# Optimization experiments

Measured on AMD Instinct MI355X. Metric: run time of the kernel, lower is better.

The kernel has to match this reference:

```python
import jax, jax.numpy as jnp
import numpy as np

B, S, D, H = 4, 2048, 1024, 16
HD = D // H  # head dim = 64


def setup_inputs() -> dict:
    key = jax.random.key(0)
    ks = jax.random.split(key, 11)
    scale = 1.0 / np.sqrt(D)
    return {
        "q": jax.random.normal(ks[0], (B, S, D), jnp.float32),
        "k": jax.random.normal(ks[1], (B, S, D), jnp.float32),
        "v": jax.random.normal(ks[2], (B, S, D), jnp.float32),
        "w_q": jax.random.normal(ks[3], (D, D), jnp.float32) * scale,
        "b_q": jax.random.normal(ks[4], (D,), jnp.float32) * scale,
        "w_k": jax.random.normal(ks[5], (D, D), jnp.float32) * scale,
        "b_k": jax.random.normal(ks[6], (D,), jnp.float32) * scale,
        "w_v": jax.random.normal(ks[7], (D, D), jnp.float32) * scale,
        "b_v": jax.random.normal(ks[8], (D,), jnp.float32) * scale,
        "w_o": jax.random.normal(ks[9], (D, D), jnp.float32) * scale,
        "b_o": jax.random.normal(ks[10], (D,), jnp.float32) * scale,
    }


def _split_heads(x):
    # [B,S,D] -> [B,H,S,HD]
    return x.reshape(B, S, H, HD).transpose(0, 2, 1, 3)


def reference(q, k, v, w_q, b_q, w_k, b_k, w_v, b_v, w_o, b_o):
    qh = _split_heads(q @ w_q + b_q)
    kh = _split_heads(k @ w_k + b_k)
    vh = _split_heads(v @ w_v + b_v)
    # full score matrix [B,H,S,S], as in the naive torch code
    score = jnp.einsum("bhqd,bhkd->bhqk", qh, kh) / jnp.sqrt(jnp.float32(HD))
    attn = jax.nn.softmax(score, axis=-1)
    out = jnp.einsum("bhqk,bhkd->bhqd", attn, vh)
    out = out.transpose(0, 2, 1, 3).reshape(B, S, D)
    return out @ w_o + b_o
```

## Files before the change

### kernel.cpp

```cpp
#include <hip/hip_runtime.h>
#include <hip/hip_bf16.h>

#define BB 4
#define SS 2048
#define DD 1024
#define HH 16
#define HDD 64
#define MM (BB*SS)

using bf16x8 = __attribute__((ext_vector_type(8))) short;
using f32x4  = __attribute__((ext_vector_type(4))) float;
using f32x16 = __attribute__((ext_vector_type(16))) float;

static __device__ __forceinline__ ushort f2bf(float f) {
    __hip_bfloat16 h = __float2bfloat16(f);
    return *reinterpret_cast<ushort*>(&h);
}

static __device__ __forceinline__ void gload_lds16(const ushort* g, ushort* l) {
    __builtin_amdgcn_global_load_lds(
        (const __attribute__((address_space(1))) unsigned int*)g,
        (__attribute__((address_space(3))) unsigned int*)l, 16, 0, 0);
}

static __device__ __forceinline__ unsigned cvtpk(float lo, float hi) {
    unsigned r;
    asm("v_cvt_pk_bf16_f32 %0, %1, %2" : "=v"(r) : "v"(lo), "v"(hi));
    return r;
}

static __device__ __forceinline__ float exp2_raw(float x) {
    float r;
    asm("v_exp_f32 %0, %1" : "=v"(r) : "v"(x));
    return r;
}

static __device__ __forceinline__ void halfswap(unsigned& a, unsigned& b, int hi) {
#if __has_builtin(__builtin_amdgcn_permlane32_swap)
    typedef int v2i __attribute__((ext_vector_type(2)));
    v2i r = __builtin_amdgcn_permlane32_swap((int)a, (int)b, false, false);
    a = (unsigned)r.x; b = (unsigned)r.y;
#else
    unsigned xa = (unsigned)__shfl_xor((int)a, 32);
    unsigned xb = (unsigned)__shfl_xor((int)b, 32);
    unsigned na = hi ? xb : a;
    unsigned nb = hi ? b : xa;
    a = na; b = nb;
#endif
}

#define PIPE_BAR(N) do {                                          \
    asm volatile("s_waitcnt vmcnt(" #N ")" ::: "memory");         \
    __builtin_amdgcn_sched_barrier(0);                            \
    __builtin_amdgcn_s_barrier();                                 \
    __builtin_amdgcn_sched_barrier(0);                            \
} while (0)

__global__ __launch_bounds__(256) void wtrans_k(
    const float* __restrict__ w0, const float* __restrict__ w1,
    const float* __restrict__ w2, const float* __restrict__ w3,
    ushort* __restrict__ o0, ushort* __restrict__ o1,
    ushort* __restrict__ o2, ushort* __restrict__ o3)
{
    __shared__ float tile[32][33];
    const float* W; ushort* O;
    switch (blockIdx.z) {
        case 0:  W = w0; O = o0; break;
        case 1:  W = w1; O = o1; break;
        case 2:  W = w2; O = o2; break;
        default: W = w3; O = o3; break;
    }
    const int tx = threadIdx.x & 31, ty = threadIdx.x >> 5;
    const int n0 = blockIdx.x * 32, k0 = blockIdx.y * 32;
    #pragma unroll
    for (int i = 0; i < 4; i++)
        tile[ty * 4 + i][tx] = W[(size_t)(k0 + ty * 4 + i) * DD + n0 + tx];
    __syncthreads();
    #pragma unroll
    for (int i = 0; i < 4; i++)
        O[(size_t)(n0 + ty * 4 + i) * DD + k0 + tx] = f2bf(tile[tx][ty * 4 + i]);
}

__global__ __launch_bounds__(256) void gemm_qkv_k(
    const float* __restrict__ qi, const float* __restrict__ ki,
    const float* __restrict__ vi,
    const ushort* __restrict__ wqT, const ushort* __restrict__ wkT,
    const ushort* __restrict__ wvT,
    const float* __restrict__ b_q, const float* __restrict__ b_k,
    const float* __restrict__ b_v,
    ushort* __restrict__ qo, ushort* __restrict__ ko, ushort* __restrict__ vo)
{
    __shared__ ushort As[128 * 40];
    __shared__ ushort Bs[128 * 32];

    const int seg = blockIdx.x >> 9;
    int bid = blockIdx.x & 511;
    bid = (bid & 7) * 64 + (bid >> 3);
    const int mt = bid >> 3, nt = bid & 7;
    const int m0 = mt * 128, n0 = nt * 128;

    const float*  A32  = seg == 0 ? qi  : seg == 1 ? ki  : vi;
    const ushort* WT   = seg == 0 ? wqT : seg == 1 ? wkT : wvT;
    const float*  bias = seg == 0 ? b_q : seg == 1 ? b_k : b_v;
    ushort*       Cout = seg == 0 ? qo  : seg == 1 ? ko  : vo;
    const float   sc   = seg == 0 ? 0.180336880111f : 1.0f;

    const int t  = threadIdx.x;
    const int w  = t >> 6;
    const int l  = t & 63;
    const int lr = l & 15;
    const int lg = l >> 4;
    const int wr = w >> 1, wc = w & 1;

    const int ar = t >> 2;
    const int ac = (t & 3) * 8;
    const int srow = l >> 2;
    const int scol = (l & 3) * 8;

    f32x4 acc[4][4];
    #pragma unroll
    for (int mi = 0; mi < 4; mi++)
        #pragma unroll
        for (int ni = 0; ni < 4; ni++)
            acc[mi][ni] = (f32x4){0.f, 0.f, 0.f, 0.f};

    const float*  Ab = A32 + (size_t)m0 * DD;
    const ushort* Bb = WT  + (size_t)n0 * DD;

    float4 a0[2], a1[2];
    #pragma unroll
    for (int j = 0; j < 2; j++) {
        const float* p = Ab + (size_t)(ar + 64 * j) * DD + ac;
        a0[j] = *(const float4*)p;
        a1[j] = *(const float4*)(p + 4);
    }

    for (int k0 = 0; k0 < DD; k0 += 32) {
        __builtin_amdgcn_s_barrier();
        #pragma unroll
        for (int j = 0; j < 2; j++) {
            union { unsigned u[4]; bf16x8 v8; } fr;
            fr.u[0] = cvtpk(a0[j].x, a0[j].y);
            fr.u[1] = cvtpk(a0[j].z, a0[j].w);
            fr.u[2] = cvtpk(a1[j].x, a1[j].y);
            fr.u[3] = cvtpk(a1[j].z, a1[j].w);
            *(bf16x8*)&As[(ar + 64 * j) * 40 + ac] = fr.v8;
        }
        #pragma unroll
        for (int j = 0; j < 2; j++) {
            const int rbase = (w * 2 + j) * 16;
            gload_lds16(Bb + (size_t)(rbase + srow) * DD + k0 + scol,
                        &Bs[rbase * 32]);
        }
        __builtin_amdgcn_sched_barrier(0);
        {
            const int kn = (k0 + 32 < DD) ? k0 + 32 : 0;
            #pragma unroll
            for (int j = 0; j < 2; j++) {
                const float* p = Ab + (size_t)(ar + 64 * j) * DD + kn + ac;
                a0[j] = *(const float4*)p;
                a1[j] = *(const float4*)(p + 4);
            }
        }
        asm volatile("s_waitcnt vmcnt(4) lgkmcnt(0)" ::: "memory");
        __builtin_amdgcn_sched_barrier(0);
        __builtin_amdgcn_s_barrier();
        __builtin_amdgcn_sched_barrier(0);

        bf16x8 af[4], bfr[4];
        #pragma unroll
        for (int mi = 0; mi < 4; mi++)
            af[mi] = *(const bf16x8*)&As[(wr * 64 + mi * 16 + lr) * 40 + lg * 8];
        #pragma unroll
        for (int ni = 0; ni < 4; ni++)
            bfr[ni] = *(const bf16x8*)&Bs[(wc * 64 + ni * 16 + lr) * 32 + lg * 8];
        #pragma unroll
        for (int mi = 0; mi < 4; mi++)
            #pragma unroll
            for (int ni = 0; ni < 4; ni++)
                acc[mi][ni] = __builtin_amdgcn_mfma_f32_16x16x32_bf16(
                    af[mi], bfr[ni], acc[mi][ni], 0, 0, 0);
    }

    #pragma unroll
    for (int mi = 0; mi < 4; mi++) {
        #pragma unroll
        for (int ni = 0; ni < 4; ni++) {
            const int c  = n0 + wc * 64 + ni * 16 + lr;
            const float bc = bias[c];
            const int r0 = m0 + wr * 64 + mi * 16 + lg * 4;
            if (seg == 2) {
                const int bi = r0 >> 11, si = r0 & 2047;
                const int hi = c >> 6,  hd = c & 63;
                ushort pk[4];
                #pragma unroll
                for (int rg = 0; rg < 4; rg++)
                    pk[rg] = f2bf(acc[mi][ni][rg] + bc);
                *(uint2*)&Cout[(((size_t)(bi * HH + hi) * HDD) + hd) * SS + si] =
                    *(const uint2*)pk;
            } else {
                #pragma unroll
                for (int rg = 0; rg < 4; rg++) {
                    const int r = r0 + rg;
                    const int bi = r >> 11, si = r & 2047;
                    const int hi = c >> 6,  hd = c & 63;
                    Cout[(((size_t)(bi * HH + hi) * SS) + si) * HDD + hd] =
                        f2bf((acc[mi][ni][rg] + bc) * sc);
                }
            }
        }
    }
}

__global__ __launch_bounds__(256) void gemm_out_k(
    const ushort* __restrict__ A, const ushort* __restrict__ WT,
    const float* __restrict__ bias, float* __restrict__ Cout)
{
    __shared__ ushort As[128 * 32];
    __shared__ ushort Bs[128 * 32];

    const int t  = threadIdx.x;
    const int w  = t >> 6;
    const int l  = t & 63;
    const int lr = l & 15;
    const int lg = l >> 4;
    const int wr = w >> 1, wc = w & 1;

    int bid = blockIdx.x;
    bid = (bid & 7) * 64 + (bid >> 3);
    const int mt = bid >> 3, nt = bid & 7;
    const int m0 = mt * 128, n0 = nt * 128;

    const int srow = l >> 2;
    const int scol = (l & 3) * 8;

    f32x4 acc[4][4];
    #pragma unroll
    for (int mi = 0; mi < 4; mi++)
        #pragma unroll
        for (int ni = 0; ni < 4; ni++)
            acc[mi][ni] = (f32x4){0.f, 0.f, 0.f, 0.f};

    const ushort* Ab = A  + (size_t)m0 * DD;
    const ushort* Bb = WT + (size_t)n0 * DD;

    for (int k0 = 0; k0 < DD; k0 += 32) {
        __syncthreads();
        #pragma unroll
        for (int j = 0; j < 2; j++) {
            const int rbase = (w * 2 + j) * 16;
            gload_lds16(Ab + (size_t)(rbase + srow) * DD + k0 + scol, &As[rbase * 32]);
            gload_lds16(Bb + (size_t)(rbase + srow) * DD + k0 + scol, &Bs[rbase * 32]);
        }
        __syncthreads();

        bf16x8 af[4], bfr[4];
        #pragma unroll
        for (int mi = 0; mi < 4; mi++)
            af[mi] = *(const bf16x8*)&As[(wr * 64 + mi * 16 + lr) * 32 + lg * 8];
        #pragma unroll
        for (int ni = 0; ni < 4; ni++)
            bfr[ni] = *(const bf16x8*)&Bs[(wc * 64 + ni * 16 + lr) * 32 + lg * 8];
        #pragma unroll
        for (int mi = 0; mi < 4; mi++)
            #pragma unroll
            for (int ni = 0; ni < 4; ni++)
                acc[mi][ni] = __builtin_amdgcn_mfma_f32_16x16x32_bf16(
                    af[mi], bfr[ni], acc[mi][ni], 0, 0, 0);
    }

    #pragma unroll
    for (int mi = 0; mi < 4; mi++) {
        #pragma unroll
        for (int ni = 0; ni < 4; ni++) {
            const int c  = n0 + wc * 64 + ni * 16 + lr;
            const float bc = bias[c];
            const int r0 = m0 + wr * 64 + mi * 16 + lg * 4;
            #pragma unroll
            for (int rg = 0; rg < 4; rg++)
                Cout[(size_t)(r0 + rg) * DD + c] = acc[mi][ni][rg] + bc;
        }
    }
}

__global__ __launch_bounds__(256, 2) void flash_attn_mfma(
    const ushort* __restrict__ qh, const ushort* __restrict__ kh,
    const ushort* __restrict__ vt, ushort* __restrict__ ctx)
{
    __shared__ ushort smem[16384];

    const int t  = threadIdx.x;
    const int w  = t >> 6;
    const int l  = t & 63;
    const int hi = l >> 5;
    const int lq = l & 31;

    const int wg = (blockIdx.x & 7) * 64 + (blockIdx.x >> 3);
    const int bi = wg >> 7;
    const int h  = (wg >> 3) & 15;
    const int q0 = (wg & 7) * 256;

    const size_t base  = (size_t)(bi * HH + h) * SS * HDD;
    const size_t basev = (size_t)(bi * HH + h) * HDD * SS;

    bf16x8 qf0[4], qf1[4];
    {
        const ushort* qp0 = qh + base + (size_t)(q0 + w * 64 + lq) * HDD;
        const ushort* qp1 = qp0 + 32 * HDD;
        #pragma unroll
        for (int ds = 0; ds < 4; ds++) {
            qf0[ds] = *(const bf16x8*)(qp0 + ds * 16 + hi * 8);
            qf1[ds] = *(const bf16x8*)(qp1 + ds * 16 + hi * 8);
        }
    }

    f32x16 o00 = {}, o01 = {}, o10 = {}, o11 = {};
    float l0 = 0.f, l1 = 0.f;

    const int rsub = l >> 3;
    const int csw  = ((l & 7) ^ rsub) * 8;
    auto stageK = [&](int buf, int kv) {
        #pragma unroll
        for (int j = 0; j < 2; j++) {
            const int rb = 16 * w + 8 * j;
            gload_lds16(kh + base + (size_t)(kv + rb + rsub) * HDD + csw,
                        &smem[buf * 4096 + rb * 64]);
        }
    };
    auto stageV = [&](int buf, int kv) {
        #pragma unroll
        for (int j = 0; j < 2; j++) {
            const int rb = 16 * w + 8 * j;
            gload_lds16(vt + basev + (size_t)(rb + rsub) * SS + kv + csw,
                        &smem[8192 + buf * 4096 + rb * 64]);
        }
    };

    auto qk2 = [&](const ushort* KB, int kvh, f32x16& sg0, f32x16& sg1) {
        sg0 = (f32x16){};
        sg1 = (f32x16){};
        __builtin_amdgcn_s_setprio(1);
        #pragma unroll
        for (int ds = 0; ds < 4; ds++) {
            const int slot = ((ds * 2 + hi) ^ (l & 7)) * 8;
            bf16x8 ka = *(const bf16x8*)&KB[(kvh * 32 + lq) * 64 + slot];
            sg0 = __builtin_amdgcn_mfma_f32_32x32x16_bf16(ka, qf0[ds], sg0, 0, 0, 0);
            sg1 = __builtin_amdgcn_mfma_f32_32x32x16_bf16(ka, qf1[ds], sg1, 0, 0, 0);
        }
        __builtin_amdgcn_s_setprio(0);
    };

    auto finish16 = [&](f32x16& s, float& lacc, bf16x8* pa2) {
        float t0 = 0.f, t1 = 0.f, t2 = 0.f, t3 = 0.f;
        #pragma unroll
        for (int r = 0; r < 16; r += 4) {
            s[r + 0] = exp2_raw(s[r + 0]); t0 += s[r + 0];
            s[r + 1] = exp2_raw(s[r + 1]); t1 += s[r + 1];
            s[r + 2] = exp2_raw(s[r + 2]); t2 += s[r + 2];
            s[r + 3] = exp2_raw(s[r + 3]); t3 += s[r + 3];
        }
        lacc += (t0 + t1) + (t2 + t3);
        #pragma unroll
        for (int sblk = 0; sblk < 2; sblk++) {
            const int ob = sblk * 8;
            unsigned a = cvtpk(s[ob + 0], s[ob + 1]);
            unsigned b = cvtpk(s[ob + 4], s[ob + 5]);
            halfswap(a, b, hi);
            unsigned c = cvtpk(s[ob + 2], s[ob + 3]);
            unsigned d = cvtpk(s[ob + 6], s[ob + 7]);
            halfswap(c, d, hi);
            union { unsigned u[4]; bf16x8 v; } fr;
            fr.u[0] = a; fr.u[1] = c; fr.u[2] = b; fr.u[3] = d;
            pa2[sblk] = fr.v;
        }
    };

    auto pvhalf = [&](const ushort* VB, int kvh,
                      const bf16x8* pg0, const bf16x8* pg1) {
        __builtin_amdgcn_s_setprio(1);
        #pragma unroll
        for (int ksl = 0; ksl < 2; ksl++) {
            const int ks = kvh * 2 + ksl;
            const int slot = ((ks * 2 + hi) ^ (l & 7)) * 8;
            bf16x8 vb0 = *(const bf16x8*)&VB[lq * 64 + slot];
            bf16x8 vb1 = *(const bf16x8*)&VB[(32 + lq) * 64 + slot];
            o00 = __builtin_amdgcn_mfma_f32_32x32x16_bf16(pg0[ksl], vb0, o00, 0, 0, 0);
            o01 = __builtin_amdgcn_mfma_f32_32x32x16_bf16(pg0[ksl], vb1, o01, 0, 0, 0);
            o10 = __builtin_amdgcn_mfma_f32_32x32x16_bf16(pg1[ksl], vb0, o10, 0, 0, 0);
            o11 = __builtin_amdgcn_mfma_f32_32x32x16_bf16(pg1[ksl], vb1, o11, 0, 0, 0);
        }
        __builtin_amdgcn_s_setprio(0);
    };

    stageK(0, 0); stageV(0, 0);
    int cur = 0;

    for (int tt = 0; tt < 32; tt++) {
        PIPE_BAR(0);
        if (tt + 1 < 32) { stageK(cur ^ 1, (tt + 1) * 64);
                           stageV(cur ^ 1, (tt + 1) * 64); }

        const ushort* KB = &smem[cur * 4096];
        const ushort* VB = &smem[8192 + cur * 4096];

        f32x16 sA, sB, sC, sD;
        qk2(KB, 0, sA, sB);
        qk2(KB, 1, sC, sD);

        bf16x8 pg0[2], pg1[2];
        finish16(sA, l0, pg0);
        finish16(sB, l1, pg1);
        pvhalf(VB, 0, pg0, pg1);
        finish16(sC, l0, pg0);
        finish16(sD, l1, pg1);
        pvhalf(VB, 1, pg0, pg1);

        cur ^= 1;
    }

    const float ls0 = l0 + __shfl_xor(l0, 32);
    const float ls1 = l1 + __shfl_xor(l1, 32);
    const float iv0 = 1.0f / ls0;
    const float iv1 = 1.0f / ls1;
    #pragma unroll
    for (int r = 0; r < 16; r++) {
        const int qq = (r & 3) + 8 * (r >> 2) + 4 * hi;
        const float a0 = __shfl(iv0, qq);
        const float a1 = __shfl(iv1, qq);
        const int row0 = q0 + w * 64 + qq;
        ushort* op0 = ctx + (size_t)(bi * SS + row0) * DD + h * HDD;
        op0[lq]      = f2bf(o00[r] * a0);
        op0[32 + lq] = f2bf(o01[r] * a0);
        ushort* op1 = op0 + (size_t)32 * DD;
        op1[lq]      = f2bf(o10[r] * a1);
        op1[32 + lq] = f2bf(o11[r] * a1);
    }
}

extern "C" void kernel_launch(void* const* d_in, const int* in_sizes, int n_in,
                              void* d_out, int out_size, void* d_ws, size_t ws_size,
                              hipStream_t stream) {
    const float* q   = (const float*)d_in[0];
    const float* k   = (const float*)d_in[1];
    const float* v   = (const float*)d_in[2];
    const float* w_q = (const float*)d_in[3];
    const float* b_q = (const float*)d_in[4];
    const float* w_k = (const float*)d_in[5];
    const float* b_k = (const float*)d_in[6];
    const float* w_v = (const float*)d_in[7];
    const float* b_v = (const float*)d_in[8];
    const float* w_o = (const float*)d_in[9];
    const float* b_o = (const float*)d_in[10];
    float* out = (float*)d_out;

    const size_t SZ = (size_t)BB * SS * DD;
    const size_t WZ = (size_t)DD * DD;
    ushort* ws2  = (ushort*)d_ws;
    ushort* qh   = ws2;
    ushort* kh   = ws2 + SZ;
    ushort* vt   = ws2 + 2 * SZ;
    ushort* ctxb = ws2 + 3 * SZ;
    ushort* wqT  = ws2 + 4 * SZ;
    ushort* wkT  = wqT + WZ;
    ushort* wvT  = wkT + WZ;
    ushort* woT  = wvT + WZ;

    wtrans_k<<<dim3(32, 32, 4), 256, 0, stream>>>(w_q, w_k, w_v, w_o,
                                                  wqT, wkT, wvT, woT);

    gemm_qkv_k<<<dim3(1536), 256, 0, stream>>>(q, k, v, wqT, wkT, wvT,
                                               b_q, b_k, b_v, qh, kh, vt);

    flash_attn_mfma<<<dim3(512), 256, 0, stream>>>(qh, kh, vt, ctxb);

    gemm_out_k<<<dim3(512), 256, 0, stream>>>(ctxb, woT, b_o, out);
}
```

Before: 182.7 us.

## Software-pipeline QK^T one tile ahead of softmax/PV with triple-buffered V

Restructures the flash-attention main loop so the QK^T MFMAs for the next KV tile are issued alongside the softmax and PV work of the current tile. V staging becomes a three-slot rotation and LDS grows to hold the extra buffer. The goal is to overlap MFMA score computation with exp/max VALU work and hide LDS latency. In exchange, the doubled score accumulators raise register pressure, which could hurt occupancy under launch_bounds(256,2) or cause spills.

```diff
diff --git a/kernel.cpp b/kernel.cpp
--- a/kernel.cpp
+++ b/kernel.cpp
@@ -287,7 +287,7 @@
     const ushort* __restrict__ qh, const ushort* __restrict__ kh,
     const ushort* __restrict__ vt, ushort* __restrict__ ctx)
 {
-    __shared__ ushort smem[16384];
+    __shared__ ushort smem[20480];
 
     const int t  = threadIdx.x;
     const int w  = t >> 6;
@@ -392,30 +392,44 @@
         __builtin_amdgcn_s_setprio(0);
     };
 
-    stageK(0, 0); stageV(0, 0);
-    int cur = 0;
-
-    for (int tt = 0; tt < 32; tt++) {
+    f32x16 sA0, sB0, sC0, sD0, sA1, sB1, sC1, sD1;
+    bf16x8 pg0[2], pg1[2];
+    int va = 0, vb = 1, vs = 2;
+
+    stageK(0, 0); stageV(va, 0);
+    PIPE_BAR(0);
+    stageK(1, 64); stageV(vb, 64);
+    qk2(&smem[0], 0, sA0, sB0);
+    qk2(&smem[0], 1, sC0, sD0);
+
+    for (int tt = 0; tt < 32; tt += 2) {
         PIPE_BAR(0);
-        if (tt + 1 < 32) { stageK(cur ^ 1, (tt + 1) * 64);
-                           stageV(cur ^ 1, (tt + 1) * 64); }
-
-        const ushort* KB = &smem[cur * 4096];
-        const ushort* VB = &smem[8192 + cur * 4096];
-
-        f32x16 sA, sB, sC, sD;
-        qk2(KB, 0, sA, sB);
-        qk2(KB, 1, sC, sD);
-
-        bf16x8 pg0[2], pg1[2];
-        finish16(sA, l0, pg0);
-        finish16(sB, l1, pg1);
-        pvhalf(VB, 0, pg0, pg1);
-        finish16(sC, l0, pg0);
-        finish16(sD, l1, pg1);
-        pvhalf(VB, 1, pg0, pg1);
-
-        cur ^= 1;
+        if (tt + 2 < 32) { stageK(0, (tt + 2) * 64); stageV(vs, (tt + 2) * 64); }
+        {
+            const ushort* KB1 = &smem[4096];
+            const ushort* VBa = &smem[8192 + va * 4096];
+            qk2(KB1, 0, sA1, sB1);
+            finish16(sA0, l0, pg0); finish16(sB0, l1, pg1);
+            pvhalf(VBa, 0, pg0, pg1);
+            qk2(KB1, 1, sC1, sD1);
+            finish16(sC0, l0, pg0); finish16(sD0, l1, pg1);
+            pvhalf(VBa, 1, pg0, pg1);
+        }
+        { const int v2 = va; va = vb; vb = vs; vs = v2; }
+
+        PIPE_BAR(0);
+        if (tt + 3 < 32) { stageK(1, (tt + 3) * 64); stageV(vs, (tt + 3) * 64); }
+        {
+            const ushort* KB0 = &smem[0];
+            const ushort* VBa = &smem[8192 + va * 4096];
+            if (tt + 2 < 32) qk2(KB0, 0, sA0, sB0);
+            finish16(sA1, l0, pg0); finish16(sB1, l1, pg1);
+            pvhalf(VBa, 0, pg0, pg1);
+            if (tt + 2 < 32) qk2(KB0, 1, sC0, sD0);
+            finish16(sC1, l0, pg0); finish16(sD1, l1, pg1);
+            pvhalf(VBa, 1, pg0, pg1);
+        }
+        { const int v2 = va; va = vb; vb = vs; vs = v2; }
     }
 
     const float ls0 = l0 + __shfl_xor(l0, 32);
```

Measured after the change: 409.7 us. 2.24x slower.

## Double-buffer weight tile in LDS and prefetch next K-slice ahead of compute

Applied to the files above, without the earlier changes.

The QKV projection GEMM now keeps two LDS buffers for the bf16 weight tile and issues the async global-to-LDS load for the next K step before the current step's MFMAs. This removes the per-iteration stall on the weight load. The A-tile mapping also changes so each thread loads 16 contiguous floats from one row instead of 8 floats from two rows. The cost is extra LDS for the second buffer and a reworked waitcnt/barrier sequence whose vmcnt ordering must stay correct.

```diff
diff --git a/kernel.cpp b/kernel.cpp
--- a/kernel.cpp
+++ b/kernel.cpp
@@ -91,7 +91,7 @@
     ushort* __restrict__ qo, ushort* __restrict__ ko, ushort* __restrict__ vo)
 {
     __shared__ ushort As[128 * 40];
-    __shared__ ushort Bs[128 * 32];
+    __shared__ ushort Bs[2 * 128 * 32];
 
     const int seg = blockIdx.x >> 9;
     int bid = blockIdx.x & 511;
@@ -112,8 +112,8 @@
     const int lg = l >> 4;
     const int wr = w >> 1, wc = w & 1;
 
-    const int ar = t >> 2;
-    const int ac = (t & 3) * 8;
+    const int ar = t >> 1;
+    const int ac = (t & 1) * 16;
     const int srow = l >> 2;
     const int scol = (l & 3) * 8;
 
@@ -127,42 +127,60 @@
     const float*  Ab = A32 + (size_t)m0 * DD;
     const ushort* Bb = WT  + (size_t)n0 * DD;
 
+    #pragma unroll
+    for (int j = 0; j < 2; j++) {
+        const int rbase = (w * 2 + j) * 16;
+        gload_lds16(Bb + (size_t)(rbase + srow) * DD + 0 + scol,
+                    &Bs[rbase * 32]);
+    }
+    __builtin_amdgcn_sched_barrier(0);
     float4 a0[2], a1[2];
     #pragma unroll
     for (int j = 0; j < 2; j++) {
-        const float* p = Ab + (size_t)(ar + 64 * j) * DD + ac;
-        a0[j] = *(const float4*)p;
-        a1[j] = *(const float4*)(p + 4);
+        const float* p = Ab + (size_t)ar * DD + ac + j * 0;
+        a0[j] = *(const float4*)(p + j * 8);
+        a1[j] = *(const float4*)(p + j * 8 + 4);
     }
 
     for (int k0 = 0; k0 < DD; k0 += 32) {
+        const int cur = (k0 >> 5) & 1;
+        asm volatile("s_waitcnt vmcnt(4)" ::: "memory");
+        __builtin_amdgcn_sched_barrier(0);
         __builtin_amdgcn_s_barrier();
-        #pragma unroll
-        for (int j = 0; j < 2; j++) {
-            union { unsigned u[4]; bf16x8 v8; } fr;
-            fr.u[0] = cvtpk(a0[j].x, a0[j].y);
-            fr.u[1] = cvtpk(a0[j].z, a0[j].w);
-            fr.u[2] = cvtpk(a1[j].x, a1[j].y);
-            fr.u[3] = cvtpk(a1[j].z, a1[j].w);
-            *(bf16x8*)&As[(ar + 64 * j) * 40 + ac] = fr.v8;
-        }
-        #pragma unroll
-        for (int j = 0; j < 2; j++) {
-            const int rbase = (w * 2 + j) * 16;
-            gload_lds16(Bb + (size_t)(rbase + srow) * DD + k0 + scol,
-                        &Bs[rbase * 32]);
+        __builtin_amdgcn_sched_barrier(0);
+
+        {
+            union { unsigned u[4]; bf16x8 v8; } f0, f1;
+            f0.u[0] = cvtpk(a0[0].x, a0[0].y);
+            f0.u[1] = cvtpk(a0[0].z, a0[0].w);
+            f0.u[2] = cvtpk(a1[0].x, a1[0].y);
+            f0.u[3] = cvtpk(a1[0].z, a1[0].w);
+            f1.u[0] = cvtpk(a0[1].x, a0[1].y);
+            f1.u[1] = cvtpk(a0[1].z, a0[1].w);
+            f1.u[2] = cvtpk(a1[1].x, a1[1].y);
+            f1.u[3] = cvtpk(a1[1].z, a1[1].w);
+            *(bf16x8*)&As[ar * 40 + ac]     = f0.v8;
+            *(bf16x8*)&As[ar * 40 + ac + 8] = f1.v8;
+        }
+        __builtin_amdgcn_sched_barrier(0);
+        if (k0 + 32 < DD) {
+            #pragma unroll
+            for (int j = 0; j < 2; j++) {
+                const int rbase = (w * 2 + j) * 16;
+                gload_lds16(Bb + (size_t)(rbase + srow) * DD + k0 + 32 + scol,
+                            &Bs[(cur ^ 1) * 4096 + rbase * 32]);
+            }
         }
         __builtin_amdgcn_sched_barrier(0);
         {
             const int kn = (k0 + 32 < DD) ? k0 + 32 : 0;
-            #pragma unroll
-            for (int j = 0; j < 2; j++) {
-                const float* p = Ab + (size_t)(ar + 64 * j) * DD + kn + ac;
-                a0[j] = *(const float4*)p;
-                a1[j] = *(const float4*)(p + 4);
-            }
-        }
-        asm volatile("s_waitcnt vmcnt(4) lgkmcnt(0)" ::: "memory");
+            const float* p = Ab + (size_t)ar * DD + kn + ac;
+            a0[0] = *(const float4*)p;
+            a1[0] = *(const float4*)(p + 4);
+            a0[1] = *(const float4*)(p + 8);
+            a1[1] = *(const float4*)(p + 12);
+        }
+        asm volatile("s_waitcnt lgkmcnt(0)" ::: "memory");
         __builtin_amdgcn_sched_barrier(0);
         __builtin_amdgcn_s_barrier();
         __builtin_amdgcn_sched_barrier(0);
@@ -173,7 +191,7 @@
             af[mi] = *(const bf16x8*)&As[(wr * 64 + mi * 16 + lr) * 40 + lg * 8];
         #pragma unroll
         for (int ni = 0; ni < 4; ni++)
-            bfr[ni] = *(const bf16x8*)&Bs[(wc * 64 + ni * 16 + lr) * 32 + lg * 8];
+            bfr[ni] = *(const bf16x8*)&Bs[cur * 4096 + (wc * 64 + ni * 16 + lr) * 32 + lg * 8];
         #pragma unroll
         for (int mi = 0; mi < 4; mi++)
             #pragma unroll
```

New measurement: 188.4 us. 1.03x slower.
